# Kernel tuning notes

Measured on AMD Instinct MI355X. Metric: run time of the kernel, lower is better.

## Reference

```python
import jax, jax.numpy as jnp
import numpy as np
from jax import lax

B, L, D_IN, D_H = 4096, 64, 256, 200


def setup_inputs() -> dict:
    key = jax.random.key(0)
    ks = jax.random.split(key, 9)
    s_in = 1.0 / np.sqrt(D_IN)
    s_cv = 1.0 / np.sqrt(D_IN * 4)
    return {
        "x": jax.random.normal(ks[0], (B, L, D_IN), dtype=jnp.float32),
        "Wq": jax.random.uniform(ks[1], (D_H, D_IN), jnp.float32, -s_in, s_in),
        "bq": jax.random.uniform(ks[2], (D_H,), jnp.float32, -s_in, s_in),
        "Wk": jax.random.uniform(ks[3], (D_H, D_IN), jnp.float32, -s_in, s_in),
        "bk": jax.random.uniform(ks[4], (D_H,), jnp.float32, -s_in, s_in),
        "Wv": jax.random.uniform(ks[5], (D_H, D_IN), jnp.float32, -s_in, s_in),
        "bv": jax.random.uniform(ks[6], (D_H,), jnp.float32, -s_in, s_in),
        "conv_w": jax.random.uniform(ks[7], (D_H, D_IN, 4), jnp.float32, -s_cv, s_cv),
        "conv_b": jax.random.uniform(ks[8], (D_H,), jnp.float32, -s_cv, s_cv),
    }


def reference(x, Wq, bq, Wk, bk, Wv, bv, conv_w, conv_b):
    # x: [B, L=64, 256]
    q = jax.nn.relu(jnp.einsum("bld,hd->blh", x, Wq) + bq)  # [B,L,200]
    k = jax.nn.relu(jnp.einsum("bld,hd->blh", x, Wk) + bk)  # relu commutes with permute
    v = jax.nn.relu(jnp.einsum("bld,hd->blh", x, Wv) + bv)
    scores = jnp.einsum("blh,bmh->blm", q, k)               # bmm(q, k^T): [B,L,L]
    soft = jax.nn.softmax(scores, axis=1)                   # NOTE: dim=1 (over queries), as in original
    self_att = jnp.einsum("blm,bmh->blh", soft, v)          # [B,L,200]
    b = x.shape[0]
    self_att = self_att.reshape(b, -1, 4, 16).mean(axis=2).reshape(b, 16, -1)  # [B,16,200]
    word_att = x.reshape(b, 256, 64)                        # [B, C=256, len=64]
    conv = lax.conv_general_dilated(
        word_att, conv_w, window_strides=(4,), padding="VALID",
        dimension_numbers=("NCH", "OIH", "NCH"))            # [B,200,16]
    conv = conv + conv_b[None, :, None]
    conv = conv.reshape(b, 16, -1)                          # raw reshape, as in original
    return conv + self_att                                  # [B,16,200]
```

## Files before the change

kernel.cpp:

```cpp
#include <hip/hip_runtime.h>

typedef _Float16 f16x8 __attribute__((ext_vector_type(8)));
typedef _Float16 f16x4 __attribute__((ext_vector_type(4)));
typedef float f32x4 __attribute__((ext_vector_type(4)));

static __device__ __forceinline__ f32x4 MFMA(f16x8 a, f16x8 b, f32x4 c) {
  return __builtin_amdgcn_mfma_f32_16x16x32_f16(a, b, c, 0, 0, 0);
}

__global__ void wcvt(const float* __restrict__ Wq, const float* __restrict__ Wk,
                     const float* __restrict__ Wv, const float* __restrict__ cw,
                     const float* __restrict__ bq, const float* __restrict__ bk,
                     const float* __restrict__ bv,
                     _Float16* __restrict__ Wb,
                     _Float16* __restrict__ Wcb,
                     float* __restrict__ biasp) {
  int gt = blockIdx.x * blockDim.x + threadIdx.x;
  int gs = gridDim.x * blockDim.x;
  const int WN = 224 * 256;
  for (int i = gt; i < WN; i += gs) {
    int n = i >> 8;
    Wb[i]          = (n < 200) ? (_Float16)Wq[i] : (_Float16)0.f;
    Wb[WN + i]     = (n < 200) ? (_Float16)Wk[i] : (_Float16)0.f;
    Wb[2 * WN + i] = (n < 200) ? (_Float16)Wv[i] : (_Float16)0.f;
  }
  for (int i = gt; i < 224 * 1024; i += gs) {
    int o = i >> 10;
    Wcb[i] = (o < 200) ? (_Float16)cw[i] : (_Float16)0.f;
  }
  for (int i = gt; i < 224; i += gs) {
    biasp[i]       = (i < 200) ? bq[i] : 0.f;
    biasp[224 + i] = (i < 200) ? bk[i] : 0.f;
    biasp[448 + i] = (i < 200) ? bv[i] : 0.f;
  }
}

__global__ __launch_bounds__(512, 4) void k1_proj_conv(
    const float* __restrict__ x, const _Float16* __restrict__ Wb,
    const _Float16* __restrict__ Wcb, const float* __restrict__ biasp,
    const float* __restrict__ convb,
    _Float16* __restrict__ Qg, _Float16* __restrict__ Kg,
    _Float16* __restrict__ Vtg, float* __restrict__ out) {
  extern __shared__ char smem[];
  _Float16* Xl = (_Float16*)smem;
  const int tid = threadIdx.x, lane = tid & 63, wave = tid >> 6;
  const int li = lane & 15, g = lane >> 4;
  const int b0 = blockIdx.x * 2;

  const float* xb = x + (size_t)b0 * 16384;
#pragma unroll
  for (int j = 0; j < 16; j++) {
    int f = tid + 512 * j;
    float4 v = ((const float4*)xb)[f];
    int bt = f >> 12, rem = f & 4095, l = rem >> 6, c4 = rem & 63;
    f16x4 h;
    h.x = (_Float16)v.x; h.y = (_Float16)v.y;
    h.z = (_Float16)v.z; h.w = (_Float16)v.w;
    *(f16x4*)(Xl + bt * 16896 + l * 264 + c4 * 4) = h;
  }
  __syncthreads();

#pragma unroll 1
  for (int i = 0; i < 7; i++) {
    int u = wave + 8 * i;
    if (u < 28) {
      int p = u / 14, nt = u % 14;
      const _Float16* wrow = Wb + p * 57344 + (nt * 16 + li) * 256 + 8 * g;
      f32x4 acc[2][4] = {};
#pragma unroll
      for (int kk = 0; kk < 8; kk++) {
        f16x8 aw = *(const f16x8*)(wrow + 32 * kk);
#pragma unroll
        for (int bt = 0; bt < 2; bt++)
#pragma unroll
          for (int mt = 0; mt < 4; mt++) {
            f16x8 bx = *(const f16x8*)(Xl + bt * 16896 + (mt * 16 + li) * 264 + 32 * kk + 8 * g);
            acc[bt][mt] = MFMA(aw, bx, acc[bt][mt]);
          }
      }
      float4 b4 = *(const float4*)(biasp + p * 224 + nt * 16 + 4 * g);
      _Float16* dst0 = (p == 0) ? Qg : Kg;
#pragma unroll
      for (int bt = 0; bt < 2; bt++) {
        _Float16* db = dst0 + (size_t)(b0 + bt) * 14336;
#pragma unroll
        for (int mt = 0; mt < 4; mt++) {
          f16x4 hv;
          {
            float v0 = acc[bt][mt][0] + b4.x; hv[0] = (_Float16)(v0 > 0.f ? v0 : 0.f);
            float v1 = acc[bt][mt][1] + b4.y; hv[1] = (_Float16)(v1 > 0.f ? v1 : 0.f);
            float v2 = acc[bt][mt][2] + b4.z; hv[2] = (_Float16)(v2 > 0.f ? v2 : 0.f);
            float v3 = acc[bt][mt][3] + b4.w; hv[3] = (_Float16)(v3 > 0.f ? v3 : 0.f);
          }
          *(f16x4*)(db + (mt * 16 + li) * 224 + nt * 16 + 4 * g) = hv;
        }
      }
    } else if (u < 42) {
      int nt = u - 28;
      const _Float16* wrow = Wb + 2 * 57344 + (nt * 16 + li) * 256 + 8 * g;
      f32x4 acc[2][4] = {};
#pragma unroll
      for (int kk = 0; kk < 8; kk++) {
        f16x8 bw = *(const f16x8*)(wrow + 32 * kk);
#pragma unroll
        for (int bt = 0; bt < 2; bt++)
#pragma unroll
          for (int mt = 0; mt < 4; mt++) {
            f16x8 ax = *(const f16x8*)(Xl + bt * 16896 + (mt * 16 + li) * 264 + 32 * kk + 8 * g);
            acc[bt][mt] = MFMA(ax, bw, acc[bt][mt]);
          }
      }
      float bias = biasp[448 + nt * 16 + li];
#pragma unroll
      for (int bt = 0; bt < 2; bt++) {
        _Float16* db = Vtg + (size_t)(b0 + bt) * 14336;
#pragma unroll
        for (int mt = 0; mt < 4; mt++) {
          f16x4 hv;
#pragma unroll
          for (int r = 0; r < 4; r++) {
            float v = acc[bt][mt][r] + bias;
            hv[r] = (_Float16)(v > 0.f ? v : 0.f);
          }
          *(f16x4*)(db + (nt * 16 + li) * 64 + mt * 16 + 4 * g) = hv;
        }
      }
    } else {
      int nt = u - 42, o = nt * 16 + li;
      const _Float16* wrow = Wcb + o * 1024 + 8 * g;
      f32x4 acc[2] = {};
#pragma unroll 4
      for (int kk = 0; kk < 32; kk++) {
        f16x8 bf = *(const f16x8*)(wrow + 32 * kk);
        int i1 = kk * 8 + 2 * g;
        int i2 = i1 + 1;
#pragma unroll
        for (int bt = 0; bt < 2; bt++) {
          const _Float16* xt = Xl + bt * 16896;
          union { f16x4 h[2]; f16x8 v; } af;
          af.h[0] = *(const f16x4*)(xt + (i1 >> 2) * 264 + ((i1 & 3) << 6) + 4 * li);
          af.h[1] = *(const f16x4*)(xt + (i2 >> 2) * 264 + ((i2 & 3) << 6) + 4 * li);
          acc[bt] = MFMA(af.v, bf, acc[bt]);
        }
      }
      if (o < 200) {
        float cb = convb[o];
#pragma unroll
        for (int bt = 0; bt < 2; bt++) {
          float4 vo;
          vo.x = acc[bt][0] + cb; vo.y = acc[bt][1] + cb;
          vo.z = acc[bt][2] + cb; vo.w = acc[bt][3] + cb;
          *(float4*)(out + (size_t)(b0 + bt) * 3200 + o * 16 + 4 * g) = vo;
        }
      }
    }
  }
}

#define K3_LDS 53024
__global__ __launch_bounds__(256, 3) void k3_attn(
    const _Float16* __restrict__ Qg, const _Float16* __restrict__ Kg,
    const _Float16* __restrict__ Vtg, float* __restrict__ out) {
  extern __shared__ char smem[];
  _Float16* Ks   = (_Float16*)smem;
  _Float16* Vt   = (_Float16*)smem;
  _Float16* Sb   = (_Float16*)(smem + 29184);
  float*    part = (float*)(smem + 38400);
  float*    Po   = (float*)(smem + 39424);

  const int b = blockIdx.x;
  const int tid = threadIdx.x, lane = tid & 63, wave = tid >> 6;
  const int li = lane & 15, g = lane >> 4;
  const size_t bb = (size_t)b * 14336;
  const int mt = wave;

  for (int i = tid; i < 3400; i += 256) Po[i] = 0.f;

#pragma unroll
  for (int i = 0; i < 7; i++) {
    int j = tid + 256 * i;
    f16x8 k = *(const f16x8*)(Kg + bb + j * 8);
    int row = j / 28, col = (j % 28) * 8;
    *(f16x8*)(Ks + row * 228 + col) = k;
  }
  f16x8 vreg[7];
#pragma unroll
  for (int i = 0; i < 7; i++)
    vreg[i] = *(const f16x8*)(Vtg + bb + (tid + 256 * i) * 8);
  f16x8 qreg[7];
#pragma unroll
  for (int kk = 0; kk < 7; kk++)
    qreg[kk] = *(const f16x8*)(Qg + bb + (mt * 16 + li) * 224 + kk * 32 + 8 * g);
  __syncthreads();

  f32x4 sacc[4] = {};
#pragma unroll
  for (int kk = 0; kk < 7; kk++) {
#pragma unroll
    for (int nt = 0; nt < 4; nt++) {
      f16x8 kb = *(const f16x8*)(Ks + (nt * 16 + li) * 228 + kk * 32 + 8 * g);
      sacc[nt] = MFMA(qreg[kk], kb, sacc[nt]);
    }
  }
  __syncthreads();

#pragma unroll
  for (int i = 0; i < 7; i++) {
    int j = tid + 256 * i;
    int h = j >> 3, c = j & 7;
    *(f16x8*)(Vt + h * 64 + ((c ^ (h & 7)) << 3)) = vreg[i];
  }

  float Mx[4];
  {
    float mx[4];
#pragma unroll
    for (int nt = 0; nt < 4; nt++) {
      float m0 = fmaxf(fmaxf(sacc[nt][0], sacc[nt][1]), fmaxf(sacc[nt][2], sacc[nt][3]));
      m0 = fmaxf(m0, __shfl_xor(m0, 16));
      m0 = fmaxf(m0, __shfl_xor(m0, 32));
      mx[nt] = m0;
    }
    if (g == 0) {
#pragma unroll
      for (int nt = 0; nt < 4; nt++) part[mt * 64 + nt * 16 + li] = mx[nt];
    }
  }
  __syncthreads();
#pragma unroll
  for (int nt = 0; nt < 4; nt++) {
    int col = nt * 16 + li;
    Mx[nt] = fmaxf(fmaxf(part[col], part[64 + col]),
                   fmaxf(part[128 + col], part[192 + col]));
  }
  __syncthreads();

  {
    float sm[4];
#pragma unroll
    for (int nt = 0; nt < 4; nt++) {
#pragma unroll
      for (int r = 0; r < 4; r++) sacc[nt][r] = __expf(sacc[nt][r] - Mx[nt]);
      float s0 = sacc[nt][0] + sacc[nt][1] + sacc[nt][2] + sacc[nt][3];
      s0 += __shfl_xor(s0, 16);
      s0 += __shfl_xor(s0, 32);
      sm[nt] = s0;
    }
    if (g == 0) {
#pragma unroll
      for (int nt = 0; nt < 4; nt++) part[mt * 64 + nt * 16 + li] = sm[nt];
    }
  }
  __syncthreads();
#pragma unroll
  for (int nt = 0; nt < 4; nt++) {
    int col = nt * 16 + li;
    float inv = 1.f / (part[col] + part[64 + col] + part[128 + col] + part[192 + col]);
#pragma unroll
    for (int r = 0; r < 4; r++)
      Sb[(mt * 16 + 4 * g + r) * 72 + col] = (_Float16)(sacc[nt][r] * inv);
  }
  __syncthreads();

  f16x8 pa[2][4];
#pragma unroll
  for (int kk = 0; kk < 2; kk++)
#pragma unroll
    for (int m2 = 0; m2 < 4; m2++)
      pa[kk][m2] = *(const f16x8*)(Sb + (m2 * 16 + li) * 72 + kk * 32 + 8 * g);

  for (int ntl = wave; ntl < 14; ntl += 4) {
    int h = ntl * 16 + li;
    f16x8 vb[2];
#pragma unroll
    for (int kk = 0; kk < 2; kk++) {
      int cm = 4 * kk + g;
      vb[kk] = *(const f16x8*)(Vt + h * 64 + ((cm ^ (h & 7)) << 3));
    }
    f32x4 pacc[4] = {};
#pragma unroll
    for (int kk = 0; kk < 2; kk++)
#pragma unroll
      for (int m2 = 0; m2 < 4; m2++)
        pacc[m2] = MFMA(pa[kk][m2], vb[kk], pacc[m2]);
    if (h < 200) {
#pragma unroll
      for (int m2 = 0; m2 < 4; m2++)
#pragma unroll
        for (int r = 0; r < 4; r++) {
          int l = m2 * 16 + 4 * g + r;
          int f = l * 200 + h;
          atomicAdd(&Po[(f >> 6) * 17 + (f & 15)], 0.25f * pacc[m2][r]);
        }
    }
  }
  __syncthreads();

  float* ob = out + (size_t)b * 3200;
  for (int t = tid; t < 3200; t += 256) {
    int c = t >> 4;
    ob[t] += Po[c * 17 + (t & 15)];
  }
}

#define FB_LDS 151296
__global__ __launch_bounds__(512, 2) void fused_fallback(
    const float* __restrict__ x, const _Float16* __restrict__ Wb,
    const _Float16* __restrict__ Wcb, const float* __restrict__ biasp,
    const float* __restrict__ convb, float* __restrict__ out) {
  extern __shared__ char smem[];
  _Float16* Xl = (_Float16*)smem;
  _Float16* Qs = (_Float16*)(smem + 33792);
  _Float16* Ks = (_Float16*)(smem + 63488);
  _Float16* Vt = (_Float16*)(smem + 93184);
  float* Sf    = (float*)(smem + 125440);
  _Float16* Sb = (_Float16*)(smem + 142080);
  float* SA    = (float*)(smem + 33792);
  float* Cv    = (float*)(smem + 125440);

  const int b = blockIdx.x;
  const int tid = threadIdx.x;
  const int lane = tid & 63;
  const int wave = tid >> 6;
  const int li = lane & 15;
  const int g = lane >> 4;

  const float* xb = x + (size_t)b * 16384;
  for (int i = tid; i < 4096; i += 512) {
    float4 v = ((const float4*)xb)[i];
    int e = i * 4;
    int l = e >> 8, d = e & 255;
    f16x4 h;
    h.x = (_Float16)v.x; h.y = (_Float16)v.y;
    h.z = (_Float16)v.z; h.w = (_Float16)v.w;
    *(f16x4*)(Xl + l * 264 + d) = h;
  }
  __syncthreads();

  for (int u = wave; u < 42; u += 8) {
    int p = u / 14, nt = u % 14;
    int n = nt * 16 + li;
    const _Float16* wrow = Wb + p * 57344 + n * 256 + 8 * g;
    f16x8 bfr[8];
#pragma unroll
    for (int kk = 0; kk < 8; kk++) bfr[kk] = *(const f16x8*)(wrow + kk * 32);
    float bias = biasp[p * 224 + n];
    for (int m = 0; m < 4; m++) {
      f32x4 acc = {0.f, 0.f, 0.f, 0.f};
      const _Float16* arow = Xl + (m * 16 + li) * 264 + 8 * g;
#pragma unroll
      for (int kk = 0; kk < 8; kk++) acc = MFMA(*(const f16x8*)(arow + kk * 32), bfr[kk], acc);
#pragma unroll
      for (int r = 0; r < 4; r++) {
        int row = m * 16 + 4 * g + r;
        float v = acc[r] + bias;
        v = v > 0.f ? v : 0.f;
        _Float16 hv = (_Float16)v;
        if (p == 0) Qs[row * 232 + n] = hv;
        else if (p == 1) Ks[row * 232 + n] = hv;
        else Vt[n * 72 + row] = hv;
      }
    }
  }
  __syncthreads();

  for (int t = wave * 2; t < wave * 2 + 2; t++) {
    int mt = t >> 2, nt = t & 3;
    f32x4 acc = {0.f, 0.f, 0.f, 0.f};
    const _Float16* qrow = Qs + (mt * 16 + li) * 232 + 8 * g;
    const _Float16* krow = Ks + (nt * 16 + li) * 232 + 8 * g;
#pragma unroll
    for (int kk = 0; kk < 7; kk++)
      acc = MFMA(*(const f16x8*)(qrow + kk * 32), *(const f16x8*)(krow + kk * 32), acc);
#pragma unroll
    for (int r = 0; r < 4; r++)
      Sf[(mt * 16 + 4 * g + r) * 65 + nt * 16 + li] = acc[r];
  }
  __syncthreads();

  {
    int m = tid >> 3, r = tid & 7;
    float vals[8];
    float mx = -1e30f;
#pragma unroll
    for (int i = 0; i < 8; i++) {
      float v = Sf[(r + 8 * i) * 65 + m];
      vals[i] = v;
      mx = fmaxf(mx, v);
    }
    mx = fmaxf(mx, __shfl_xor(mx, 1));
    mx = fmaxf(mx, __shfl_xor(mx, 2));
    mx = fmaxf(mx, __shfl_xor(mx, 4));
    float s = 0.f;
#pragma unroll
    for (int i = 0; i < 8; i++) { vals[i] = __expf(vals[i] - mx); s += vals[i]; }
    s += __shfl_xor(s, 1);
    s += __shfl_xor(s, 2);
    s += __shfl_xor(s, 4);
    float inv = 1.0f / s;
#pragma unroll
    for (int i = 0; i < 8; i++)
      Sb[(r + 8 * i) * 72 + m] = (_Float16)(vals[i] * inv);
  }
  __syncthreads();

  for (int nt = wave; nt < 14; nt += 8) {
    int o = nt * 16 + li;
    const _Float16* wrow = Wcb + o * 1024 + 8 * g;
    f32x4 acc = {0.f, 0.f, 0.f, 0.f};
#pragma unroll 4
    for (int kk = 0; kk < 32; kk++) {
      int i1 = kk * 8 + 2 * g;
      int i2 = i1 + 1;
      union { f16x4 h[2]; f16x8 v; } af;
      af.h[0] = *(const f16x4*)(Xl + (i1 >> 2) * 264 + ((i1 & 3) << 6) + 4 * li);
      af.h[1] = *(const f16x4*)(Xl + (i2 >> 2) * 264 + ((i2 & 3) << 6) + 4 * li);
      acc = MFMA(af.v, *(const f16x8*)(wrow + 32 * kk), acc);
    }
#pragma unroll
    for (int r = 0; r < 4; r++) Cv[(4 * g + r) * 226 + o] = acc[r];
  }

  for (int t = wave; t < 56; t += 8) {
    int mt = t / 14, nt = t % 14;
    f32x4 acc = {0.f, 0.f, 0.f, 0.f};
    const _Float16* arow = Sb + (mt * 16 + li) * 72 + 8 * g;
    const _Float16* brow = Vt + (nt * 16 + li) * 72 + 8 * g;
#pragma unroll
    for (int kk = 0; kk < 2; kk++)
      acc = MFMA(*(const f16x8*)(arow + kk * 32), *(const f16x8*)(brow + kk * 32), acc);
#pragma unroll
    for (int r = 0; r < 4; r++)
      SA[(mt * 16 + 4 * g + r) * 228 + (nt * 16 + li)] = acc[r];
  }
  __syncthreads();

  float* ob = out + (size_t)b * 3200;
  for (int t = tid; t < 3200; t += 512) {
    int c = t >> 4, s = t & 15;
    float cv = Cv[s * 226 + c] + convb[c];
    float pool = 0.f;
#pragma unroll
    for (int j = 0; j < 4; j++) {
      int flat = c * 64 + j * 16 + s;
      int l = flat / 200;
      int h = flat - l * 200;
      pool += SA[l * 228 + h];
    }
    ob[t] = cv + 0.25f * pool;
  }
}

extern "C" void kernel_launch(void* const* d_in, const int* in_sizes, int n_in,
                              void* d_out, int out_size, void* d_ws, size_t ws_size,
                              hipStream_t stream) {
  const float* x  = (const float*)d_in[0];
  const float* Wq = (const float*)d_in[1];
  const float* bq = (const float*)d_in[2];
  const float* Wk = (const float*)d_in[3];
  const float* bk = (const float*)d_in[4];
  const float* Wv = (const float*)d_in[5];
  const float* bv = (const float*)d_in[6];
  const float* cw = (const float*)d_in[7];
  const float* cb = (const float*)d_in[8];

  char* ws = (char*)d_ws;
  _Float16* Wb  = (_Float16*)ws;
  _Float16* Wcb = (_Float16*)(ws + 344064);
  float* biasp  = (float*)(ws + 802816);

  hipLaunchKernelGGL(wcvt, dim3(512), dim3(256), 0, stream,
                     Wq, Wk, Wv, cw, bq, bk, bv, Wb, Wcb, biasp);

  const size_t QKV_BASE = 805888ull;
  const size_t QKV_ONE  = 117440512ull;
  const size_t NEED = QKV_BASE + 3ull * QKV_ONE;

  if (ws_size >= NEED) {
    _Float16* Qg  = (_Float16*)(ws + QKV_BASE);
    _Float16* Kg  = (_Float16*)(ws + QKV_BASE + QKV_ONE);
    _Float16* Vtg = (_Float16*)(ws + QKV_BASE + 2 * QKV_ONE);

    hipFuncSetAttribute((const void*)k1_proj_conv,
                        hipFuncAttributeMaxDynamicSharedMemorySize, 67584);
    hipLaunchKernelGGL(k1_proj_conv, dim3(2048), dim3(512), 67584, stream,
                       x, Wb, Wcb, biasp, cb, Qg, Kg, Vtg, (float*)d_out);

    hipFuncSetAttribute((const void*)k3_attn,
                        hipFuncAttributeMaxDynamicSharedMemorySize, K3_LDS);
    hipLaunchKernelGGL(k3_attn, dim3(4096), dim3(256), K3_LDS, stream,
                       Qg, Kg, Vtg, (float*)d_out);
  } else {
    hipFuncSetAttribute((const void*)fused_fallback,
                        hipFuncAttributeMaxDynamicSharedMemorySize, FB_LDS);
    hipLaunchKernelGGL(fused_fallback, dim3(4096), dim3(512), FB_LDS, stream,
                       x, Wb, Wcb, biasp, cb, (float*)d_out);
  }
}
```

Baseline: 617.6 us.

## Make attention kernel persistent with register prefetch of next batch

The attention kernel now launches a fixed grid of 768 blocks that loop over batches, loading the next batch's Q, K and V into registers while the current batch is computed, so global load latency overlaps with compute. The two-pass softmax max/sum reduction is merged into one pass that rescales per-wave partial sums, which removes a barrier round. Syncthreads are replaced by a custom barrier macro. The changes add register pressure and a persistent-loop structure that could lower occupancy.

```diff
diff --git a/kernel.cpp b/kernel.cpp
--- a/kernel.cpp
+++ b/kernel.cpp
@@ -7,6 +7,13 @@
 static __device__ __forceinline__ f32x4 MFMA(f16x8 a, f16x8 b, f32x4 c) {
   return __builtin_amdgcn_mfma_f32_16x16x32_f16(a, b, c, 0, 0, 0);
 }
+
+#define BAR()                                          \
+  do {                                                 \
+    asm volatile("s_waitcnt lgkmcnt(0)" ::: "memory"); \
+    __builtin_amdgcn_s_barrier();                      \
+    __builtin_amdgcn_sched_barrier(0);                 \
+  } while (0)
 
 __global__ void wcvt(const float* __restrict__ Wq, const float* __restrict__ Wk,
                      const float* __restrict__ Wv, const float* __restrict__ cw,
@@ -157,7 +164,8 @@
   }
 }
 
-#define K3_LDS 53024
+#define K3_LDS 54048
+#define K3_GRID 768
 __global__ __launch_bounds__(256, 3) void k3_attn(
     const _Float16* __restrict__ Qg, const _Float16* __restrict__ Kg,
     const _Float16* __restrict__ Vtg, float* __restrict__ out) {
@@ -166,140 +174,155 @@
   _Float16* Vt   = (_Float16*)smem;
   _Float16* Sb   = (_Float16*)(smem + 29184);
   float*    part = (float*)(smem + 38400);
-  float*    Po   = (float*)(smem + 39424);
-
-  const int b = blockIdx.x;
+  float*    Po   = (float*)(smem + 40448);
+
   const int tid = threadIdx.x, lane = tid & 63, wave = tid >> 6;
   const int li = lane & 15, g = lane >> 4;
-  const size_t bb = (size_t)b * 14336;
   const int mt = wave;
 
   for (int i = tid; i < 3400; i += 256) Po[i] = 0.f;
 
-#pragma unroll
-  for (int i = 0; i < 7; i++) {
-    int j = tid + 256 * i;
-    f16x8 k = *(const f16x8*)(Kg + bb + j * 8);
-    int row = j / 28, col = (j % 28) * 8;
-    *(f16x8*)(Ks + row * 228 + col) = k;
-  }
-  f16x8 vreg[7];
+  int b = blockIdx.x;
+  size_t bb = (size_t)b * 14336;
+  f16x8 kreg[7], vreg[7], qreg[7];
+#pragma unroll
+  for (int i = 0; i < 7; i++)
+    kreg[i] = *(const f16x8*)(Kg + bb + (tid + 256 * i) * 8);
 #pragma unroll
   for (int i = 0; i < 7; i++)
     vreg[i] = *(const f16x8*)(Vtg + bb + (tid + 256 * i) * 8);
-  f16x8 qreg[7];
 #pragma unroll
   for (int kk = 0; kk < 7; kk++)
     qreg[kk] = *(const f16x8*)(Qg + bb + (mt * 16 + li) * 224 + kk * 32 + 8 * g);
-  __syncthreads();
-
-  f32x4 sacc[4] = {};
-#pragma unroll
-  for (int kk = 0; kk < 7; kk++) {
+
+#pragma unroll 1
+  for (; b < 4096; b += K3_GRID) {
+    const size_t bbn = (size_t)(b + K3_GRID) * 14336;
+    const bool pf = (b + K3_GRID) < 4096;
+
+#pragma unroll
+    for (int i = 0; i < 7; i++) {
+      int j = tid + 256 * i;
+      *(f16x8*)(Ks + (j / 28) * 228 + (j % 28) * 8) = kreg[i];
+    }
+    if (pf) {
+#pragma unroll
+      for (int i = 0; i < 7; i++)
+        kreg[i] = *(const f16x8*)(Kg + bbn + (tid + 256 * i) * 8);
+    }
+    BAR();
+
+    f32x4 sacc[4] = {};
+#pragma unroll
+    for (int kk = 0; kk < 7; kk++) {
+#pragma unroll
+      for (int nt = 0; nt < 4; nt++) {
+        f16x8 kb = *(const f16x8*)(Ks + (nt * 16 + li) * 228 + kk * 32 + 8 * g);
+        sacc[nt] = MFMA(qreg[kk], kb, sacc[nt]);
+      }
+    }
+    if (pf) {
+#pragma unroll
+      for (int kk = 0; kk < 7; kk++)
+        qreg[kk] = *(const f16x8*)(Qg + bbn + (mt * 16 + li) * 224 + kk * 32 + 8 * g);
+    }
+    BAR();
+
+#pragma unroll
+    for (int i = 0; i < 7; i++) {
+      int j = tid + 256 * i;
+      int h = j >> 3, c = j & 7;
+      *(f16x8*)(Vt + h * 64 + ((c ^ (h & 7)) << 3)) = vreg[i];
+    }
+    if (pf) {
+#pragma unroll
+      for (int i = 0; i < 7; i++)
+        vreg[i] = *(const f16x8*)(Vtg + bbn + (tid + 256 * i) * 8);
+    }
+
+    float mw[4];
 #pragma unroll
     for (int nt = 0; nt < 4; nt++) {
-      f16x8 kb = *(const f16x8*)(Ks + (nt * 16 + li) * 228 + kk * 32 + 8 * g);
-      sacc[nt] = MFMA(qreg[kk], kb, sacc[nt]);
-    }
-  }
-  __syncthreads();
-
-#pragma unroll
-  for (int i = 0; i < 7; i++) {
-    int j = tid + 256 * i;
-    int h = j >> 3, c = j & 7;
-    *(f16x8*)(Vt + h * 64 + ((c ^ (h & 7)) << 3)) = vreg[i];
-  }
-
-  float Mx[4];
-  {
-    float mx[4];
-#pragma unroll
-    for (int nt = 0; nt < 4; nt++) {
-      float m0 = fmaxf(fmaxf(sacc[nt][0], sacc[nt][1]), fmaxf(sacc[nt][2], sacc[nt][3]));
+      float m0 = fmaxf(fmaxf(sacc[nt][0], sacc[nt][1]),
+                       fmaxf(sacc[nt][2], sacc[nt][3]));
       m0 = fmaxf(m0, __shfl_xor(m0, 16));
       m0 = fmaxf(m0, __shfl_xor(m0, 32));
-      mx[nt] = m0;
-    }
-    if (g == 0) {
-#pragma unroll
-      for (int nt = 0; nt < 4; nt++) part[mt * 64 + nt * 16 + li] = mx[nt];
-    }
-  }
-  __syncthreads();
-#pragma unroll
-  for (int nt = 0; nt < 4; nt++) {
-    int col = nt * 16 + li;
-    Mx[nt] = fmaxf(fmaxf(part[col], part[64 + col]),
-                   fmaxf(part[128 + col], part[192 + col]));
-  }
-  __syncthreads();
-
-  {
-    float sm[4];
-#pragma unroll
-    for (int nt = 0; nt < 4; nt++) {
-#pragma unroll
-      for (int r = 0; r < 4; r++) sacc[nt][r] = __expf(sacc[nt][r] - Mx[nt]);
+      mw[nt] = m0;
+#pragma unroll
+      for (int r = 0; r < 4; r++) sacc[nt][r] = __expf(sacc[nt][r] - m0);
       float s0 = sacc[nt][0] + sacc[nt][1] + sacc[nt][2] + sacc[nt][3];
       s0 += __shfl_xor(s0, 16);
       s0 += __shfl_xor(s0, 32);
-      sm[nt] = s0;
-    }
-    if (g == 0) {
-#pragma unroll
-      for (int nt = 0; nt < 4; nt++) part[mt * 64 + nt * 16 + li] = sm[nt];
-    }
-  }
-  __syncthreads();
-#pragma unroll
-  for (int nt = 0; nt < 4; nt++) {
-    int col = nt * 16 + li;
-    float inv = 1.f / (part[col] + part[64 + col] + part[128 + col] + part[192 + col]);
-#pragma unroll
-    for (int r = 0; r < 4; r++)
-      Sb[(mt * 16 + 4 * g + r) * 72 + col] = (_Float16)(sacc[nt][r] * inv);
-  }
-  __syncthreads();
-
-  f16x8 pa[2][4];
-#pragma unroll
-  for (int kk = 0; kk < 2; kk++)
-#pragma unroll
-    for (int m2 = 0; m2 < 4; m2++)
-      pa[kk][m2] = *(const f16x8*)(Sb + (m2 * 16 + li) * 72 + kk * 32 + 8 * g);
-
-  for (int ntl = wave; ntl < 14; ntl += 4) {
-    int h = ntl * 16 + li;
-    f16x8 vb[2];
-#pragma unroll
-    for (int kk = 0; kk < 2; kk++) {
-      int cm = 4 * kk + g;
-      vb[kk] = *(const f16x8*)(Vt + h * 64 + ((cm ^ (h & 7)) << 3));
-    }
-    f32x4 pacc[4] = {};
+      if (g == 0) {
+        part[wave * 64 + nt * 16 + li] = m0;
+        part[256 + wave * 64 + nt * 16 + li] = s0;
+      }
+    }
+    BAR();
+
+#pragma unroll
+    for (int nt = 0; nt < 4; nt++) {
+      int col = nt * 16 + li;
+      float m0 = part[col], m1 = part[64 + col];
+      float m2 = part[128 + col], m3 = part[192 + col];
+      float M = fmaxf(fmaxf(m0, m1), fmaxf(m2, m3));
+      float S = part[256 + col] * __expf(m0 - M) +
+                part[320 + col] * __expf(m1 - M) +
+                part[384 + col] * __expf(m2 - M) +
+                part[448 + col] * __expf(m3 - M);
+      float scale = __expf(mw[nt] - M) / S;
+#pragma unroll
+      for (int r = 0; r < 4; r++)
+        Sb[(mt * 16 + 4 * g + r) * 72 + col] = (_Float16)(sacc[nt][r] * scale);
+    }
+    BAR();
+
+    f16x8 pa[2][4];
 #pragma unroll
     for (int kk = 0; kk < 2; kk++)
 #pragma unroll
       for (int m2 = 0; m2 < 4; m2++)
-        pacc[m2] = MFMA(pa[kk][m2], vb[kk], pacc[m2]);
-    if (h < 200) {
-#pragma unroll
-      for (int m2 = 0; m2 < 4; m2++)
-#pragma unroll
-        for (int r = 0; r < 4; r++) {
-          int l = m2 * 16 + 4 * g + r;
-          int f = l * 200 + h;
-          atomicAdd(&Po[(f >> 6) * 17 + (f & 15)], 0.25f * pacc[m2][r]);
-        }
-    }
-  }
-  __syncthreads();
-
-  float* ob = out + (size_t)b * 3200;
-  for (int t = tid; t < 3200; t += 256) {
-    int c = t >> 4;
-    ob[t] += Po[c * 17 + (t & 15)];
+        pa[kk][m2] = *(const f16x8*)(Sb + (m2 * 16 + li) * 72 + kk * 32 + 8 * g);
+
+#pragma unroll 1
+    for (int ntl = wave; ntl < 14; ntl += 4) {
+      int h = ntl * 16 + li;
+      f16x8 vb[2];
+#pragma unroll
+      for (int kk = 0; kk < 2; kk++) {
+        int cm = 4 * kk + g;
+        vb[kk] = *(const f16x8*)(Vt + h * 64 + ((cm ^ (h & 7)) << 3));
+      }
+      f32x4 pacc[4] = {};
+#pragma unroll
+      for (int kk = 0; kk < 2; kk++)
+#pragma unroll
+        for (int m2 = 0; m2 < 4; m2++)
+          pacc[m2] = MFMA(pa[kk][m2], vb[kk], pacc[m2]);
+      if (h < 200) {
+#pragma unroll
+        for (int m2 = 0; m2 < 4; m2++)
+#pragma unroll
+          for (int r = 0; r < 4; r++) {
+            int l = m2 * 16 + 4 * g + r;
+            int f = l * 200 + h;
+            atomicAdd(&Po[(f >> 6) * 17 + (f & 15)], 0.25f * pacc[m2][r]);
+          }
+      }
+    }
+    BAR();
+
+    {
+      float* ob = out + (size_t)b * 3200;
+#pragma unroll 1
+      for (int t = tid; t < 3200; t += 256) {
+        int idx = (t >> 4) * 17 + (t & 15);
+        float v = Po[idx];
+        Po[idx] = 0.f;
+        ob[t] += v;
+      }
+    }
+    BAR();
   }
 }
 
@@ -488,7 +511,7 @@
 
     hipFuncSetAttribute((const void*)k3_attn,
                         hipFuncAttributeMaxDynamicSharedMemorySize, K3_LDS);
-    hipLaunchKernelGGL(k3_attn, dim3(4096), dim3(256), K3_LDS, stream,
+    hipLaunchKernelGGL(k3_attn, dim3(K3_GRID), dim3(256), K3_LDS, stream,
                        Qg, Kg, Vtg, (float*)d_out);
   } else {
     hipFuncSetAttribute((const void*)fused_fallback,
```

New measurement: 783.7 us. 1.27x slower.

## Read K and V directly from global memory, merge softmax passes, raise occupancy

Applied to the files above, without the earlier changes.

The attention kernel no longer stages K and V in LDS. MFMA operands are loaded straight from global memory, which shrinks LDS use per block and lets launch bounds ask for six blocks per CU instead of three. The separate max and sum reduction passes are fused into a single pass using per-wave partial maxima and rescaled partial sums, which removes two barriers. The trade-off is uncoalesced, repeated global or L2 reads of K and V fragments in place of shared-memory reuse, plus higher register pressure under the tighter launch bound.

```diff
diff --git a/kernel.cpp b/kernel.cpp
--- a/kernel.cpp
+++ b/kernel.cpp
@@ -157,16 +157,14 @@
   }
 }
 
-#define K3_LDS 53024
-__global__ __launch_bounds__(256, 3) void k3_attn(
+#define K3_LDS 24864
+__global__ __launch_bounds__(256, 6) void k3_attn(
     const _Float16* __restrict__ Qg, const _Float16* __restrict__ Kg,
     const _Float16* __restrict__ Vtg, float* __restrict__ out) {
   extern __shared__ char smem[];
-  _Float16* Ks   = (_Float16*)smem;
-  _Float16* Vt   = (_Float16*)smem;
-  _Float16* Sb   = (_Float16*)(smem + 29184);
-  float*    part = (float*)(smem + 38400);
-  float*    Po   = (float*)(smem + 39424);
+  _Float16* Sb   = (_Float16*)smem;
+  float*    part = (float*)(smem + 9216);
+  float*    Po   = (float*)(smem + 11264);
 
   const int b = blockIdx.x;
   const int tid = threadIdx.x, lane = tid & 63, wave = tid >> 6;
@@ -176,89 +174,55 @@
 
   for (int i = tid; i < 3400; i += 256) Po[i] = 0.f;
 
-#pragma unroll
-  for (int i = 0; i < 7; i++) {
-    int j = tid + 256 * i;
-    f16x8 k = *(const f16x8*)(Kg + bb + j * 8);
-    int row = j / 28, col = (j % 28) * 8;
-    *(f16x8*)(Ks + row * 228 + col) = k;
-  }
-  f16x8 vreg[7];
-#pragma unroll
-  for (int i = 0; i < 7; i++)
-    vreg[i] = *(const f16x8*)(Vtg + bb + (tid + 256 * i) * 8);
   f16x8 qreg[7];
 #pragma unroll
   for (int kk = 0; kk < 7; kk++)
     qreg[kk] = *(const f16x8*)(Qg + bb + (mt * 16 + li) * 224 + kk * 32 + 8 * g);
-  __syncthreads();
 
   f32x4 sacc[4] = {};
 #pragma unroll
   for (int kk = 0; kk < 7; kk++) {
 #pragma unroll
     for (int nt = 0; nt < 4; nt++) {
-      f16x8 kb = *(const f16x8*)(Ks + (nt * 16 + li) * 228 + kk * 32 + 8 * g);
+      f16x8 kb = *(const f16x8*)(Kg + bb + (nt * 16 + li) * 224 + kk * 32 + 8 * g);
       sacc[nt] = MFMA(qreg[kk], kb, sacc[nt]);
     }
   }
-  __syncthreads();
-
-#pragma unroll
-  for (int i = 0; i < 7; i++) {
-    int j = tid + 256 * i;
-    int h = j >> 3, c = j & 7;
-    *(f16x8*)(Vt + h * 64 + ((c ^ (h & 7)) << 3)) = vreg[i];
-  }
-
-  float Mx[4];
-  {
-    float mx[4];
-#pragma unroll
-    for (int nt = 0; nt < 4; nt++) {
-      float m0 = fmaxf(fmaxf(sacc[nt][0], sacc[nt][1]), fmaxf(sacc[nt][2], sacc[nt][3]));
-      m0 = fmaxf(m0, __shfl_xor(m0, 16));
-      m0 = fmaxf(m0, __shfl_xor(m0, 32));
-      mx[nt] = m0;
-    }
+
+  float mw[4];
+#pragma unroll
+  for (int nt = 0; nt < 4; nt++) {
+    float m0 = fmaxf(fmaxf(sacc[nt][0], sacc[nt][1]),
+                     fmaxf(sacc[nt][2], sacc[nt][3]));
+    m0 = fmaxf(m0, __shfl_xor(m0, 16));
+    m0 = fmaxf(m0, __shfl_xor(m0, 32));
+    mw[nt] = m0;
+#pragma unroll
+    for (int r = 0; r < 4; r++) sacc[nt][r] = __expf(sacc[nt][r] - m0);
+    float s0 = sacc[nt][0] + sacc[nt][1] + sacc[nt][2] + sacc[nt][3];
+    s0 += __shfl_xor(s0, 16);
+    s0 += __shfl_xor(s0, 32);
     if (g == 0) {
-#pragma unroll
-      for (int nt = 0; nt < 4; nt++) part[mt * 64 + nt * 16 + li] = mx[nt];
-    }
-  }
-  __syncthreads();
+      part[wave * 64 + nt * 16 + li] = m0;
+      part[256 + wave * 64 + nt * 16 + li] = s0;
+    }
+  }
+  __syncthreads();
+
 #pragma unroll
   for (int nt = 0; nt < 4; nt++) {
     int col = nt * 16 + li;
-    Mx[nt] = fmaxf(fmaxf(part[col], part[64 + col]),
-                   fmaxf(part[128 + col], part[192 + col]));
-  }
-  __syncthreads();
-
-  {
-    float sm[4];
-#pragma unroll
-    for (int nt = 0; nt < 4; nt++) {
-#pragma unroll
-      for (int r = 0; r < 4; r++) sacc[nt][r] = __expf(sacc[nt][r] - Mx[nt]);
-      float s0 = sacc[nt][0] + sacc[nt][1] + sacc[nt][2] + sacc[nt][3];
-      s0 += __shfl_xor(s0, 16);
-      s0 += __shfl_xor(s0, 32);
-      sm[nt] = s0;
-    }
-    if (g == 0) {
-#pragma unroll
-      for (int nt = 0; nt < 4; nt++) part[mt * 64 + nt * 16 + li] = sm[nt];
-    }
-  }
-  __syncthreads();
-#pragma unroll
-  for (int nt = 0; nt < 4; nt++) {
-    int col = nt * 16 + li;
-    float inv = 1.f / (part[col] + part[64 + col] + part[128 + col] + part[192 + col]);
+    float m0 = part[col], m1 = part[64 + col];
+    float m2 = part[128 + col], m3 = part[192 + col];
+    float M = fmaxf(fmaxf(m0, m1), fmaxf(m2, m3));
+    float S = part[256 + col] * __expf(m0 - M) +
+              part[320 + col] * __expf(m1 - M) +
+              part[384 + col] * __expf(m2 - M) +
+              part[448 + col] * __expf(m3 - M);
+    float scale = __expf(mw[nt] - M) / S;
 #pragma unroll
     for (int r = 0; r < 4; r++)
-      Sb[(mt * 16 + 4 * g + r) * 72 + col] = (_Float16)(sacc[nt][r] * inv);
+      Sb[(mt * 16 + 4 * g + r) * 72 + col] = (_Float16)(sacc[nt][r] * scale);
   }
   __syncthreads();
 
@@ -269,14 +233,13 @@
     for (int m2 = 0; m2 < 4; m2++)
       pa[kk][m2] = *(const f16x8*)(Sb + (m2 * 16 + li) * 72 + kk * 32 + 8 * g);
 
+#pragma unroll 1
   for (int ntl = wave; ntl < 14; ntl += 4) {
     int h = ntl * 16 + li;
     f16x8 vb[2];
 #pragma unroll
-    for (int kk = 0; kk < 2; kk++) {
-      int cm = 4 * kk + g;
-      vb[kk] = *(const f16x8*)(Vt + h * 64 + ((cm ^ (h & 7)) << 3));
-    }
+    for (int kk = 0; kk < 2; kk++)
+      vb[kk] = *(const f16x8*)(Vtg + bb + h * 64 + kk * 32 + 8 * g);
     f32x4 pacc[4] = {};
 #pragma unroll
     for (int kk = 0; kk < 2; kk++)
```

Measured after the change: 570.9 us. 1.08x faster.
